# Kernel optimization log

Measured on AMD Instinct MI355X. Metric: run time of the kernel, lower is better.

## Reference

```python
import jax, jax.numpy as jnp
import numpy as np

N, F, H, D, E, G = 50000, 64, 4, 64, 800000, 64
NEG_SLOPE = 0.2


def setup_inputs() -> dict:
    key = jax.random.key(0)
    ks = jax.random.split(key, 10)
    return {
        "x": jax.random.normal(ks[0], (N, F), jnp.float32),
        "mask": jax.random.uniform(ks[1], (N, F), jnp.float32),
        "edge_index": jax.random.randint(ks[2], (2, E), 0, N, jnp.int64),
        "batch_idx": jnp.sort(jax.random.randint(ks[3], (N,), 0, G, jnp.int64)),
        "W_gat": jax.random.normal(ks[4], (H * D, F), jnp.float32) * 0.05,
        "att_src": jax.random.normal(ks[5], (H, D), jnp.float32) * 0.05,
        "att_dst": jax.random.normal(ks[6], (H, D), jnp.float32) * 0.05,
        "bias_gat": jax.random.normal(ks[7], (H * D,), jnp.float32) * 0.05,
        "W_lin": jax.random.normal(ks[8], (D, H * D), jnp.float32) * 0.05,
        "b_lin": jax.random.normal(ks[9], (D,), jnp.float32) * 0.05,
    }


def reference(x, mask, edge_index, batch_idx, W_gat, att_src, att_dst, bias_gat, W_lin, b_lin):
    n = x.shape[0]
    row, col = edge_index[0], edge_index[1]

    # ---- get_mask(mask, edge_index, hops=1): scatter_add(mask[col] -> row), threshold
    m = jax.ops.segment_sum(mask[col], row, num_segments=n)
    m = (m > 0).astype(x.dtype)  # [N, F]

    # ---- GATConv(x, edge_index): add self loops (PyG default)
    loop = jnp.arange(n, dtype=edge_index.dtype)
    src = jnp.concatenate([edge_index[0], loop])  # source j
    dst = jnp.concatenate([edge_index[1], loop])  # target i

    xw = (x @ W_gat.T).reshape(n, H, D)  # per-head projection [N,H,D]
    a_s = jnp.einsum("nhd,hd->nh", xw, att_src)  # [N,H]
    a_d = jnp.einsum("nhd,hd->nh", xw, att_dst)
    e = jax.nn.leaky_relu(a_s[src] + a_d[dst], NEG_SLOPE)  # [E+N, H]

    # segment softmax over incoming edges of each destination node
    emax = jax.ops.segment_max(e, dst, num_segments=n)  # [N,H]
    ex = jnp.exp(e - emax[dst])
    denom = jax.ops.segment_sum(ex, dst, num_segments=n)
    alpha = ex / (denom[dst] + 1e-16)  # [E+N, H]

    out = jax.ops.segment_sum(alpha[:, :, None] * xw[src], dst, num_segments=n)
    out = out.reshape(n, H * D) + bias_gat  # concat heads + bias

    # ---- mask expand to heads and fuse: x = linear(x * mask)
    mexp = jnp.broadcast_to(m[:, None, :], (n, H, F)).reshape(n, H * F)
    out = (out * mexp) @ W_lin.T + b_lin  # [N, D]

    # ---- GraphSizeNorm: divide by sqrt(#nodes in each graph)
    deg = jax.ops.segment_sum(jnp.ones((n,), x.dtype), batch_idx, num_segments=G)
    inv_sqrt = jnp.where(deg > 0, deg, 1.0) ** -0.5
    out = out * inv_sqrt[batch_idx][:, None]
    return out
```

## Files before the change

kernel.cpp:

```cpp
#include <hip/hip_runtime.h>
#include <cstdint>
#include <math.h>

constexpr float NEG_SLOPE = 0.2f;

__device__ __forceinline__ float lrelu(float v) { return v > 0.0f ? v : NEG_SLOPE * v; }

__device__ __forceinline__ unsigned short f2bf(float f) {
    uint32_t u = __float_as_uint(f);
    uint32_t r = (u + 0x7fffu + ((u >> 16) & 1u)) >> 16;
    return (unsigned short)r;
}
__device__ __forceinline__ float bf2f(unsigned short v) { return __uint_as_float((uint32_t)v << 16); }
__device__ __forceinline__ float bflo(uint32_t v) { return __uint_as_float(v << 16); }
__device__ __forceinline__ float bfhi(uint32_t v) { return __uint_as_float(v & 0xffff0000u); }

typedef short bf16x8 __attribute__((ext_vector_type(8)));
typedef float f32x4 __attribute__((ext_vector_type(4)));

__launch_bounds__(256)
__global__ void k_att2z(const float* __restrict__ x, const float* __restrict__ Wg,
                        const float* __restrict__ att_s, const float* __restrict__ att_d,
                        float* __restrict__ a_s, float* __restrict__ a_d,
                        int* __restrict__ deg, unsigned long long* __restrict__ magg,
                        int* __restrict__ startg, int N)
{
    __shared__ float vs_l[256];
    __shared__ float vd_l[256];
    int tid = threadIdx.x;
    {
        int h = tid >> 6, k = tid & 63;
        float s = 0.f, d = 0.f;
        for (int dd = 0; dd < 64; ++dd) {
            float w = Wg[(size_t)(h * 64 + dd) * 64 + k];
            s += w * att_s[h * 64 + dd];
            d += w * att_d[h * 64 + dd];
        }
        vs_l[tid] = s; vd_l[tid] = d;
    }
    if (blockIdx.x == 0 && tid < 64) startg[tid] = N;
    __syncthreads();
    int i = blockIdx.x * 256 + tid;
    if (i >= N) return;
    deg[i] = 0; magg[i] = 0ULL;
    const float4* xr = (const float4*)(x + (size_t)i * 64);
    float s0=0,s1=0,s2=0,s3=0, d0=0,d1=0,d2=0,d3=0;
    #pragma unroll
    for (int q = 0; q < 16; ++q) {
        float4 xv = xr[q];
        float4 a0 = *(const float4*)&vs_l[4*q];
        float4 a1 = *(const float4*)&vs_l[64 + 4*q];
        float4 a2 = *(const float4*)&vs_l[128 + 4*q];
        float4 a3 = *(const float4*)&vs_l[192 + 4*q];
        float4 c0 = *(const float4*)&vd_l[4*q];
        float4 c1 = *(const float4*)&vd_l[64 + 4*q];
        float4 c2 = *(const float4*)&vd_l[128 + 4*q];
        float4 c3 = *(const float4*)&vd_l[192 + 4*q];
        s0 += xv.x*a0.x + xv.y*a0.y + xv.z*a0.z + xv.w*a0.w;
        s1 += xv.x*a1.x + xv.y*a1.y + xv.z*a1.z + xv.w*a1.w;
        s2 += xv.x*a2.x + xv.y*a2.y + xv.z*a2.z + xv.w*a2.w;
        s3 += xv.x*a3.x + xv.y*a3.y + xv.z*a3.z + xv.w*a3.w;
        d0 += xv.x*c0.x + xv.y*c0.y + xv.z*c0.z + xv.w*c0.w;
        d1 += xv.x*c1.x + xv.y*c1.y + xv.z*c1.z + xv.w*c1.w;
        d2 += xv.x*c2.x + xv.y*c2.y + xv.z*c2.z + xv.w*c2.w;
        d3 += xv.x*c3.x + xv.y*c3.y + xv.z*c3.z + xv.w*c3.w;
    }
    *(float4*)&a_s[(size_t)i * 4] = make_float4(s0, s1, s2, s3);
    *(float4*)&a_d[(size_t)i * 4] = make_float4(d0, d1, d2, d3);
}

__global__ void k_maskdeg(const float* __restrict__ mask, const int* __restrict__ ei,
                          unsigned long long* __restrict__ mbits, int* __restrict__ deg,
                          int N, int E, int nbMask)
{
    int tid = threadIdx.x;
    if ((int)blockIdx.x < nbMask) {
        int wid  = (blockIdx.x * 256 + tid) >> 6;
        int lane = tid & 63;
        if (wid >= N) return;
        float v = mask[(size_t)wid * 64 + lane];
        unsigned long long b = __ballot(v > 0.0f);
        if (lane == 0) mbits[wid] = b;
    } else {
        int e = (blockIdx.x - nbMask) * 256 + tid;
        if (e >= E) return;
        atomicAdd(deg + ei[E + e], 1);
    }
}

__launch_bounds__(256)
__global__ void k_gemm1m(const float* __restrict__ x, const float* __restrict__ Wg,
                         const int* __restrict__ batch_idx,
                         uint32_t* __restrict__ xwp, int* __restrict__ startg, int N)
{
    __shared__ __align__(16) uint32_t AsH[2048];
    __shared__ __align__(16) uint32_t AsL[2048];
    __shared__ __align__(16) uint32_t BsH[8192];
    const int tid = threadIdx.x;
    const int r0  = blockIdx.x * 64;

    for (int idx = tid; idx < 2048; idx += 256) {
        int r = idx >> 5, k2 = idx & 31;
        float2 v = make_float2(0.f, 0.f);
        if (r0 + r < N) v = *(const float2*)&x[(size_t)(r0 + r) * 64 + 2 * k2];
        unsigned short h0 = f2bf(v.x), h1 = f2bf(v.y);
        unsigned short l0 = f2bf(v.x - bf2f(h0)), l1 = f2bf(v.y - bf2f(h1));
        int di = (r * 32 + k2) ^ ((r & 7) << 2);
        AsH[di] = (uint32_t)h0 | ((uint32_t)h1 << 16);
        AsL[di] = (uint32_t)l0 | ((uint32_t)l1 << 16);
    }
    for (int idx = tid; idx < 8192; idx += 256) {
        int c = idx >> 5, k2 = idx & 31;
        float2 v = *(const float2*)&Wg[(size_t)c * 64 + 2 * k2];
        int di = (c * 32 + k2) ^ ((c & 7) << 2);
        BsH[di] = (uint32_t)f2bf(v.x) | ((uint32_t)f2bf(v.y) << 16);
    }
    if (tid < 64 && (r0 + tid) < N) {
        int i = r0 + tid;
        int b = batch_idx[i];
        int pb = (i > 0) ? batch_idx[i - 1] : -1;
        if (b != pb) startg[b] = i;
    }
    __syncthreads();

    const int lane = tid & 63;
    const int wv   = tid >> 6;
    const int rl   = lane & 15;
    const int kg   = lane >> 4;
    const int ct0  = (wv & 1) * 2 + (wv >> 1) * 8;
    const int swz  = (rl & 7) << 2;

    f32x4 acc[4][4];
    #pragma unroll
    for (int r = 0; r < 4; ++r)
        #pragma unroll
        for (int cs = 0; cs < 4; ++cs) acc[r][cs] = (f32x4){0.f, 0.f, 0.f, 0.f};

    #pragma unroll
    for (int ks = 0; ks < 2; ++ks) {
        bf16x8 aH[4], aL[4], bH[4];
        #pragma unroll
        for (int r = 0; r < 4; ++r) {
            int ui = (((r * 16 + rl) * 32) + ks * 16 + kg * 4) ^ swz;
            aH[r] = *(const bf16x8*)&AsH[ui];
            aL[r] = *(const bf16x8*)&AsL[ui];
        }
        #pragma unroll
        for (int cs = 0; cs < 4; ++cs) {
            int ct = ct0 + (cs & 1) + (cs >> 1) * 4;
            int ui = (((ct * 16 + rl) * 32) + ks * 16 + kg * 4) ^ swz;
            bH[cs] = *(const bf16x8*)&BsH[ui];
        }
        #pragma unroll
        for (int r = 0; r < 4; ++r)
            #pragma unroll
            for (int cs = 0; cs < 4; ++cs) {
                acc[r][cs] = __builtin_amdgcn_mfma_f32_16x16x32_bf16(aH[r], bH[cs], acc[r][cs], 0, 0, 0);
                acc[r][cs] = __builtin_amdgcn_mfma_f32_16x16x32_bf16(aL[r], bH[cs], acc[r][cs], 0, 0, 0);
            }
    }

    #pragma unroll
    for (int r = 0; r < 4; ++r) {
        #pragma unroll
        for (int reg = 0; reg < 4; ++reg) {
            int row = r0 + r * 16 + kg * 4 + reg;
            if (row < N) {
                #pragma unroll
                for (int p = 0; p < 2; ++p) {
                    int c_lo = (ct0 + p) * 16 + rl;
                    int wrd  = ((c_lo >> 7) << 6) | (c_lo & 63);
                    uint32_t lo = f2bf(acc[r][p][reg]);
                    uint32_t hi = f2bf(acc[r][p + 2][reg]);
                    xwp[(size_t)row * 128 + wrd] = lo | (hi << 16);
                }
            }
        }
    }
}

__global__ void k_scan1(const int* __restrict__ deg, int* __restrict__ off,
                        int* __restrict__ bsum, int N)
{
    __shared__ int s[256];
    int t = threadIdx.x;
    int i = blockIdx.x * 256 + t;
    int v = (i < N) ? deg[i] : 0;
    s[t] = v; __syncthreads();
    for (int o = 1; o < 256; o <<= 1) {
        int u = (t >= o) ? s[t - o] : 0;
        __syncthreads();
        s[t] += u;
        __syncthreads();
    }
    int incl = s[t];
    if (i < N) off[i] = incl - v;
    if (t == 255) bsum[blockIdx.x] = incl;
}

__global__ void k_scan2(const int* __restrict__ bsum, int* __restrict__ bpre,
                        int* __restrict__ off, const int* __restrict__ startg,
                        float* __restrict__ invs, int NB, int N)
{
    __shared__ int s[256];
    int t = threadIdx.x;
    int v = (t < NB) ? bsum[t] : 0;
    s[t] = v; __syncthreads();
    for (int o = 1; o < 256; o <<= 1) {
        int u = (t >= o) ? s[t - o] : 0;
        __syncthreads();
        s[t] += u;
        __syncthreads();
    }
    if (t < NB) bpre[t] = s[t] - v;
    if (t == 255) off[N] = s[255];
    if (t < 64) {
        int st = startg[t];
        int en = N;
        for (int g2 = t + 1; g2 < 64; ++g2) en = min(en, startg[g2]);
        int d = en - st;
        float dv = (d > 0) ? (float)d : 1.0f;
        invs[t] = 1.0f / sqrtf(dv);
    }
}

__global__ void k_scan3(int* __restrict__ off, int* __restrict__ cursor,
                        const int* __restrict__ bpre, int N)
{
    int i = blockIdx.x * blockDim.x + threadIdx.x;
    if (i >= N) return;
    int v = off[i] + bpre[blockIdx.x];
    off[i] = v;
    cursor[i] = v;
}

__global__ void k_fill(const int* __restrict__ ei, int* __restrict__ cursor,
                       int* __restrict__ csr,
                       const unsigned long long* __restrict__ mbits,
                       unsigned long long* __restrict__ magg, int E)
{
    int e = blockIdx.x * blockDim.x + threadIdx.x;
    if (e >= E) return;
    int r = ei[e];
    int c = ei[E + e];
    unsigned long long b = mbits[c];
    if ((magg[r] & b) != b) atomicOr(magg + r, b);
    int pos = atomicAdd(cursor + c, 1);
    csr[pos] = r;
}

__launch_bounds__(256)
__global__ void k_main7(const uint32_t* __restrict__ xwp,
                        const float* __restrict__ a_s,
                        const float* __restrict__ a_d,
                        const int* __restrict__ off,
                        const int* __restrict__ csr,
                        const unsigned long long* __restrict__ magg,
                        const float* __restrict__ bias,
                        uint32_t* __restrict__ tbp, int N)
{
    __shared__ __align__(16) uint32_t su[4][64];
    __shared__ __align__(16) float2 e01s[4][64];
    __shared__ __align__(16) float2 e23s[4][64];

    const int lane = threadIdx.x & 63;
    const int wv   = threadIdx.x >> 6;
    const int wid  = blockIdx.x * 4 + wv;
    const int nw   = gridDim.x * 4;
    const int hp   = lane >> 5;
    const int d0   = (lane & 31) * 2;

    const uint2* xw2 = (const uint2*)xwp;
    const float2 bsL = *(const float2*)&bias[hp * 128 + d0];
    const float2 bsH = *(const float2*)&bias[hp * 128 + 64 + d0];
    const float2* ep = hp ? e23s[wv] : e01s[wv];

    for (int i = wid; i < N; i += nw) {
        const int beg = off[i], end = off[i + 1];
        const float4 adv = *(const float4*)(a_d + (size_t)i * 4);
        const float4 asv = *(const float4*)(a_s + (size_t)i * 4);
        const float ex0 = __expf(lrelu(asv.x + adv.x));
        const float ex1 = __expf(lrelu(asv.y + adv.y));
        const float ex2 = __expf(lrelu(asv.z + adv.z));
        const float ex3 = __expf(lrelu(asv.w + adv.w));

        const uint2 sv = xw2[(size_t)i * 64 + lane];
        const float wls = hp ? ex2 : ex0;
        const float whs = hp ? ex3 : ex1;
        float accL0 = wls * bflo(sv.x), accH0 = whs * bfhi(sv.x);
        float accL1 = wls * bflo(sv.y), accH1 = whs * bfhi(sv.y);
        float sL = 0.f, sH = 0.f;

        for (int kc = beg; kc < end; kc += 64) {
            const int cnt = min(64, end - kc);
            uint32_t sreg = 0; float e0 = 0.f, e1 = 0.f, e2 = 0.f, e3 = 0.f;
            if (lane < cnt) {
                sreg = csr[kc + lane];
                const float4 g = *(const float4*)(a_s + (size_t)sreg * 4);
                e0 = __expf(lrelu(g.x + adv.x));
                e1 = __expf(lrelu(g.y + adv.y));
                e2 = __expf(lrelu(g.z + adv.z));
                e3 = __expf(lrelu(g.w + adv.w));
            }
            su[wv][lane]   = sreg;
            e01s[wv][lane] = make_float2(e0, e1);
            e23s[wv][lane] = make_float2(e2, e3);

            int j = 0;
            for (; j + 8 <= cnt; j += 8) {
                uint4 sq0 = *(const uint4*)&su[wv][j];
                uint4 sq1 = *(const uint4*)&su[wv][j + 4];
                float2 w0 = ep[j],   w1 = ep[j+1], w2 = ep[j+2], w3 = ep[j+3];
                float2 w4 = ep[j+4], w5 = ep[j+5], w6 = ep[j+6], w7 = ep[j+7];
                uint2 v0 = xw2[(size_t)sq0.x * 64 + lane];
                uint2 v1 = xw2[(size_t)sq0.y * 64 + lane];
                uint2 v2 = xw2[(size_t)sq0.z * 64 + lane];
                uint2 v3 = xw2[(size_t)sq0.w * 64 + lane];
                uint2 v4 = xw2[(size_t)sq1.x * 64 + lane];
                uint2 v5 = xw2[(size_t)sq1.y * 64 + lane];
                uint2 v6 = xw2[(size_t)sq1.z * 64 + lane];
                uint2 v7 = xw2[(size_t)sq1.w * 64 + lane];
                sL += w0.x + w1.x + w2.x + w3.x + w4.x + w5.x + w6.x + w7.x;
                sH += w0.y + w1.y + w2.y + w3.y + w4.y + w5.y + w6.y + w7.y;
                accL0 += w0.x * bflo(v0.x); accH0 += w0.y * bfhi(v0.x);
                accL1 += w0.x * bflo(v0.y); accH1 += w0.y * bfhi(v0.y);
                accL0 += w1.x * bflo(v1.x); accH0 += w1.y * bfhi(v1.x);
                accL1 += w1.x * bflo(v1.y); accH1 += w1.y * bfhi(v1.y);
                accL0 += w2.x * bflo(v2.x); accH0 += w2.y * bfhi(v2.x);
                accL1 += w2.x * bflo(v2.y); accH1 += w2.y * bfhi(v2.y);
                accL0 += w3.x * bflo(v3.x); accH0 += w3.y * bfhi(v3.x);
                accL1 += w3.x * bflo(v3.y); accH1 += w3.y * bfhi(v3.y);
                accL0 += w4.x * bflo(v4.x); accH0 += w4.y * bfhi(v4.x);
                accL1 += w4.x * bflo(v4.y); accH1 += w4.y * bfhi(v4.y);
                accL0 += w5.x * bflo(v5.x); accH0 += w5.y * bfhi(v5.x);
                accL1 += w5.x * bflo(v5.y); accH1 += w5.y * bfhi(v5.y);
                accL0 += w6.x * bflo(v6.x); accH0 += w6.y * bfhi(v6.x);
                accL1 += w6.x * bflo(v6.y); accH1 += w6.y * bfhi(v6.y);
                accL0 += w7.x * bflo(v7.x); accH0 += w7.y * bfhi(v7.x);
                accL1 += w7.x * bflo(v7.y); accH1 += w7.y * bfhi(v7.y);
            }
            for (; j + 4 <= cnt; j += 4) {
                uint4 sq = *(const uint4*)&su[wv][j];
                float2 wA = ep[j], wB = ep[j+1], wC = ep[j+2], wD = ep[j+3];
                uint2 vA = xw2[(size_t)sq.x * 64 + lane];
                uint2 vB = xw2[(size_t)sq.y * 64 + lane];
                uint2 vC = xw2[(size_t)sq.z * 64 + lane];
                uint2 vD = xw2[(size_t)sq.w * 64 + lane];
                sL += wA.x + wB.x + wC.x + wD.x;
                sH += wA.y + wB.y + wC.y + wD.y;
                accL0 += wA.x * bflo(vA.x); accH0 += wA.y * bfhi(vA.x);
                accL1 += wA.x * bflo(vA.y); accH1 += wA.y * bfhi(vA.y);
                accL0 += wB.x * bflo(vB.x); accH0 += wB.y * bfhi(vB.x);
                accL1 += wB.x * bflo(vB.y); accH1 += wB.y * bfhi(vB.y);
                accL0 += wC.x * bflo(vC.x); accH0 += wC.y * bfhi(vC.x);
                accL1 += wC.x * bflo(vC.y); accH1 += wC.y * bfhi(vC.y);
                accL0 += wD.x * bflo(vD.x); accH0 += wD.y * bfhi(vD.x);
                accL1 += wD.x * bflo(vD.y); accH1 += wD.y * bfhi(vD.y);
            }
            for (; j < cnt; ++j) {
                uint32_t s = su[wv][j];
                float2 wE = ep[j];
                uint2 v = xw2[(size_t)s * 64 + lane];
                sL += wE.x; sH += wE.y;
                accL0 += wE.x * bflo(v.x); accH0 += wE.y * bfhi(v.x);
                accL1 += wE.x * bflo(v.y); accH1 += wE.y * bfhi(v.y);
            }
        }
        const float rlo = 1.0f / (sL + wls + 1e-16f);
        const float rhi = 1.0f / (sH + whs + 1e-16f);

        const unsigned long long mb = magg[i];
        const float m0 = (float)((mb >> d0) & 1ULL);
        const float m1 = (float)((mb >> (d0 + 1)) & 1ULL);
        float oL0 = (accL0 * rlo + bsL.x) * m0, oL1 = (accL1 * rlo + bsL.y) * m1;
        float oH0 = (accH0 * rhi + bsH.x) * m0, oH1 = (accH1 * rhi + bsH.y) * m1;
        tbp[(size_t)i * 128 + hp * 64 + (lane & 31)]      = (uint32_t)f2bf(oL0) | ((uint32_t)f2bf(oL1) << 16);
        tbp[(size_t)i * 128 + hp * 64 + 32 + (lane & 31)] = (uint32_t)f2bf(oH0) | ((uint32_t)f2bf(oH1) << 16);
    }
}

__launch_bounds__(256)
__global__ void k_gemm2m(const uint32_t* __restrict__ tbp, const float* __restrict__ Wl,
                         const float* __restrict__ bl,
                         const int* __restrict__ batch_idx, const float* __restrict__ invs,
                         float* __restrict__ out, int N)
{
    __shared__ __align__(16) uint32_t AH[2048];
    __shared__ __align__(16) uint32_t BH[2048];
    __shared__ __align__(16) uint32_t BL[2048];
    const int tid = threadIdx.x;
    const int r0  = blockIdx.x * 64;
    const int lane = tid & 63;
    const int wv   = tid >> 6;
    const int rl   = lane & 15;
    const int kg   = lane >> 4;
    const int swz  = (rl & 7) << 2;

    f32x4 acc[4];
    #pragma unroll
    for (int r = 0; r < 4; ++r) acc[r] = (f32x4){0.f, 0.f, 0.f, 0.f};

    for (int kc = 0; kc < 4; ++kc) {
        if (kc) __syncthreads();
        for (int idx = tid; idx < 2048; idx += 256) {
            int r = idx >> 5, k2 = idx & 31;
            uint32_t v = 0;
            if (r0 + r < N) v = tbp[(size_t)(r0 + r) * 128 + kc * 32 + k2];
            AH[(r * 32 + k2) ^ ((r & 7) << 2)] = v;
        }
        for (int idx = tid; idx < 2048; idx += 256) {
            int c = idx >> 5, k2 = idx & 31;
            float2 v = *(const float2*)&Wl[(size_t)c * 256 + kc * 64 + 2 * k2];
            unsigned short h0 = f2bf(v.x), h1 = f2bf(v.y);
            unsigned short l0 = f2bf(v.x - bf2f(h0)), l1 = f2bf(v.y - bf2f(h1));
            int di = (c * 32 + k2) ^ ((c & 7) << 2);
            BH[di] = (uint32_t)h0 | ((uint32_t)h1 << 16);
            BL[di] = (uint32_t)l0 | ((uint32_t)l1 << 16);
        }
        __syncthreads();

        #pragma unroll
        for (int ks = 0; ks < 2; ++ks) {
            int uib = ((wv * 16 + rl) * 32 + ks * 16 + kg * 4) ^ swz;
            bf16x8 bHf = *(const bf16x8*)&BH[uib];
            bf16x8 bLf = *(const bf16x8*)&BL[uib];
            #pragma unroll
            for (int r = 0; r < 4; ++r) {
                int ui = ((r * 16 + rl) * 32 + ks * 16 + kg * 4) ^ swz;
                bf16x8 aHf = *(const bf16x8*)&AH[ui];
                acc[r] = __builtin_amdgcn_mfma_f32_16x16x32_bf16(aHf, bHf, acc[r], 0, 0, 0);
                acc[r] = __builtin_amdgcn_mfma_f32_16x16x32_bf16(aHf, bLf, acc[r], 0, 0, 0);
            }
        }
    }

    const int col = wv * 16 + rl;
    const float blc = bl[col];
    #pragma unroll
    for (int r = 0; r < 4; ++r) {
        #pragma unroll
        for (int reg = 0; reg < 4; ++reg) {
            int row = r0 + r * 16 + kg * 4 + reg;
            if (row < N) {
                float sc = invs[batch_idx[row]];
                out[(size_t)row * 64 + col] = (acc[r][reg] + blc) * sc;
            }
        }
    }
}

extern "C" void kernel_launch(void* const* d_in, const int* in_sizes, int n_in,
                              void* d_out, int out_size, void* d_ws, size_t ws_size,
                              hipStream_t stream)
{
    const float* x      = (const float*)d_in[0];
    const float* mask   = (const float*)d_in[1];
    const int*   ei     = (const int*)d_in[2];
    const int*   batch  = (const int*)d_in[3];
    const float* Wg     = (const float*)d_in[4];
    const float* att_s  = (const float*)d_in[5];
    const float* att_d  = (const float*)d_in[6];
    const float* bias_g = (const float*)d_in[7];
    const float* Wl     = (const float*)d_in[8];
    const float* bl     = (const float*)d_in[9];
    float* out = (float*)d_out;

    const int N = in_sizes[0] / 64;
    const int E = in_sizes[2] / 2;

    char* w = (char*)d_ws;
    auto alloc = [&](size_t bytes) { char* p = w; w += (bytes + 255) & ~(size_t)255; return p; };
    uint32_t* xwp  = (uint32_t*)alloc((size_t)N * 128 * 4);
    uint32_t* tbp  = (uint32_t*)alloc((size_t)N * 128 * 4);
    float* a_s   = (float*)alloc((size_t)N * 4 * 4);
    float* a_d   = (float*)alloc((size_t)N * 4 * 4);
    unsigned long long* mbits = (unsigned long long*)alloc((size_t)N * 8);
    unsigned long long* magg  = (unsigned long long*)alloc((size_t)N * 8);
    int* deg    = (int*)alloc((size_t)N * 4);
    int* off    = (int*)alloc((size_t)(N + 1) * 4);
    int* cursor = (int*)alloc((size_t)N * 4);
    int* csr    = (int*)alloc((size_t)E * 4);
    int* bsum   = (int*)alloc(256 * 4);
    int* bpre   = (int*)alloc(256 * 4);
    int* startg = (int*)alloc(64 * 4);
    float* invs = (float*)alloc(64 * 4);

    int nbN4  = (N + 3) / 4;
    int nbE   = (E + 255) / 256;
    int nb256 = (N + 255) / 256;

    k_att2z<<<nb256, 256, 0, stream>>>(x, Wg, att_s, att_d, a_s, a_d, deg, magg, startg, N);
    k_maskdeg<<<nbN4 + nbE, 256, 0, stream>>>(mask, ei, mbits, deg, N, E, nbN4);
    k_gemm1m<<<(N + 63) / 64, 256, 0, stream>>>(x, Wg, batch, xwp, startg, N);
    k_scan1<<<nb256, 256, 0, stream>>>(deg, off, bsum, N);
    k_scan2<<<1, 256, 0, stream>>>(bsum, bpre, off, startg, invs, nb256, N);
    k_scan3<<<nb256, 256, 0, stream>>>(off, cursor, bpre, N);
    k_fill<<<nbE, 256, 0, stream>>>(ei, cursor, csr, mbits, magg, E);
    k_main7<<<2048, 256, 0, stream>>>(xwp, a_s, a_d, off, csr, magg, bias_g, tbp, N);
    k_gemm2m<<<(N + 63) / 64, 256, 0, stream>>>(tbp, Wl, bl, batch, invs, out, N);
}
```

Baseline: 234.6 us.

## Precompute bf16 weights once and fold attention logits into first GEMM

```diff
diff --git a/kernel.cpp b/kernel.cpp
--- a/kernel.cpp
+++ b/kernel.cpp
@@ -18,17 +18,30 @@
 typedef short bf16x8 __attribute__((ext_vector_type(8)));
 typedef float f32x4 __attribute__((ext_vector_type(4)));
 
-__launch_bounds__(256)
-__global__ void k_att2z(const float* __restrict__ x, const float* __restrict__ Wg,
+__global__ void k_wprep(const float* __restrict__ Wg, const float* __restrict__ Wl,
                         const float* __restrict__ att_s, const float* __restrict__ att_d,
-                        float* __restrict__ a_s, float* __restrict__ a_d,
-                        int* __restrict__ deg, unsigned long long* __restrict__ magg,
+                        uint32_t* __restrict__ WgB, uint32_t* __restrict__ WlH,
+                        uint32_t* __restrict__ WlL, uint32_t* __restrict__ attB,
                         int* __restrict__ startg, int N)
 {
-    __shared__ float vs_l[256];
-    __shared__ float vd_l[256];
-    int tid = threadIdx.x;
-    {
+    const int tid = threadIdx.x;
+    if (blockIdx.x == 0) {
+        for (int w = tid; w < 8192; w += 256) {
+            int c = w >> 5, k2 = w & 31;
+            float2 v = *(const float2*)&Wg[(size_t)c * 64 + 2 * k2];
+            WgB[w] = (uint32_t)f2bf(v.x) | ((uint32_t)f2bf(v.y) << 16);
+        }
+    } else if (blockIdx.x == 1) {
+        for (int w = tid; w < 8192; w += 256) {
+            int c = w >> 7, k2 = w & 127;
+            float2 v = *(const float2*)&Wl[(size_t)c * 256 + 2 * k2];
+            unsigned short h0 = f2bf(v.x), h1 = f2bf(v.y);
+            unsigned short l0 = f2bf(v.x - bf2f(h0)), l1 = f2bf(v.y - bf2f(h1));
+            WlH[w] = (uint32_t)h0 | ((uint32_t)h1 << 16);
+            WlL[w] = (uint32_t)l0 | ((uint32_t)l1 << 16);
+        }
+    } else {
+        __shared__ float vs_l[256], vd_l[256];
         int h = tid >> 6, k = tid & 63;
         float s = 0.f, d = 0.f;
         for (int dd = 0; dd < 64; ++dd) {
@@ -37,36 +50,20 @@
             d += w * att_d[h * 64 + dd];
         }
         vs_l[tid] = s; vd_l[tid] = d;
-    }
-    if (blockIdx.x == 0 && tid < 64) startg[tid] = N;
-    __syncthreads();
-    int i = blockIdx.x * 256 + tid;
-    if (i >= N) return;
-    deg[i] = 0; magg[i] = 0ULL;
-    const float4* xr = (const float4*)(x + (size_t)i * 64);
-    float s0=0,s1=0,s2=0,s3=0, d0=0,d1=0,d2=0,d3=0;
-    #pragma unroll
-    for (int q = 0; q < 16; ++q) {
-        float4 xv = xr[q];
-        float4 a0 = *(const float4*)&vs_l[4*q];
-        float4 a1 = *(const float4*)&vs_l[64 + 4*q];
-        float4 a2 = *(const float4*)&vs_l[128 + 4*q];
-        float4 a3 = *(const float4*)&vs_l[192 + 4*q];
-        float4 c0 = *(const float4*)&vd_l[4*q];
-        float4 c1 = *(const float4*)&vd_l[64 + 4*q];
-        float4 c2 = *(const float4*)&vd_l[128 + 4*q];
-        float4 c3 = *(const float4*)&vd_l[192 + 4*q];
-        s0 += xv.x*a0.x + xv.y*a0.y + xv.z*a0.z + xv.w*a0.w;
-        s1 += xv.x*a1.x + xv.y*a1.y + xv.z*a1.z + xv.w*a1.w;
-        s2 += xv.x*a2.x + xv.y*a2.y + xv.z*a2.z + xv.w*a2.w;
-        s3 += xv.x*a3.x + xv.y*a3.y + xv.z*a3.z + xv.w*a3.w;
-        d0 += xv.x*c0.x + xv.y*c0.y + xv.z*c0.z + xv.w*c0.w;
-        d1 += xv.x*c1.x + xv.y*c1.y + xv.z*c1.z + xv.w*c1.w;
-        d2 += xv.x*c2.x + xv.y*c2.y + xv.z*c2.z + xv.w*c2.w;
-        d3 += xv.x*c3.x + xv.y*c3.y + xv.z*c3.z + xv.w*c3.w;
-    }
-    *(float4*)&a_s[(size_t)i * 4] = make_float4(s0, s1, s2, s3);
-    *(float4*)&a_d[(size_t)i * 4] = make_float4(d0, d1, d2, d3);
+        if (tid < 64) startg[tid] = N;
+        __syncthreads();
+        for (int w = tid; w < 512; w += 256) {
+            int col = w >> 5, k2 = w & 31;
+            int hh = col & 3;
+            int plane = (col >> 2) & 1;
+            const float* buf = (col >> 3) ? vd_l : vs_l;
+            float v0 = buf[hh * 64 + 2 * k2];
+            float v1 = buf[hh * 64 + 2 * k2 + 1];
+            unsigned short h0 = f2bf(v0), h1 = f2bf(v1);
+            if (plane) { h0 = f2bf(v0 - bf2f(h0)); h1 = f2bf(v1 - bf2f(h1)); }
+            attB[w] = (uint32_t)h0 | ((uint32_t)h1 << 16);
+        }
+    }
 }
 
 __global__ void k_maskdeg(const float* __restrict__ mask, const int* __restrict__ ei,
@@ -89,13 +86,13 @@
 }
 
 __launch_bounds__(256)
-__global__ void k_gemm1m(const float* __restrict__ x, const float* __restrict__ Wg,
-                         const int* __restrict__ batch_idx,
-                         uint32_t* __restrict__ xwp, int* __restrict__ startg, int N)
+__global__ void k_gemm1n(const float* __restrict__ x, const uint32_t* __restrict__ WgB,
+                         const uint32_t* __restrict__ attB, const int* __restrict__ batch_idx,
+                         uint32_t* __restrict__ xwp, float* __restrict__ a_s,
+                         float* __restrict__ a_d, int* __restrict__ startg, int N)
 {
     __shared__ __align__(16) uint32_t AsH[2048];
     __shared__ __align__(16) uint32_t AsL[2048];
-    __shared__ __align__(16) uint32_t BsH[8192];
     const int tid = threadIdx.x;
     const int r0  = blockIdx.x * 64;
 
@@ -109,12 +106,6 @@
         AsH[di] = (uint32_t)h0 | ((uint32_t)h1 << 16);
         AsL[di] = (uint32_t)l0 | ((uint32_t)l1 << 16);
     }
-    for (int idx = tid; idx < 8192; idx += 256) {
-        int c = idx >> 5, k2 = idx & 31;
-        float2 v = *(const float2*)&Wg[(size_t)c * 64 + 2 * k2];
-        int di = (c * 32 + k2) ^ ((c & 7) << 2);
-        BsH[di] = (uint32_t)f2bf(v.x) | ((uint32_t)f2bf(v.y) << 16);
-    }
     if (tid < 64 && (r0 + tid) < N) {
         int i = r0 + tid;
         int b = batch_idx[i];
@@ -135,6 +126,7 @@
     for (int r = 0; r < 4; ++r)
         #pragma unroll
         for (int cs = 0; cs < 4; ++cs) acc[r][cs] = (f32x4){0.f, 0.f, 0.f, 0.f};
+    f32x4 accA = (f32x4){0.f, 0.f, 0.f, 0.f};
 
     #pragma unroll
     for (int ks = 0; ks < 2; ++ks) {
@@ -148,9 +140,9 @@
         #pragma unroll
         for (int cs = 0; cs < 4; ++cs) {
             int ct = ct0 + (cs & 1) + (cs >> 1) * 4;
-            int ui = (((ct * 16 + rl) * 32) + ks * 16 + kg * 4) ^ swz;
-            bH[cs] = *(const bf16x8*)&BsH[ui];
-        }
+            bH[cs] = *(const bf16x8*)(WgB + ((ct * 16 + rl) * 32 + ks * 16 + kg * 4));
+        }
+        bf16x8 bAtt = *(const bf16x8*)(attB + (rl * 32 + ks * 16 + kg * 4));
         #pragma unroll
         for (int r = 0; r < 4; ++r)
             #pragma unroll
@@ -158,6 +150,8 @@
                 acc[r][cs] = __builtin_amdgcn_mfma_f32_16x16x32_bf16(aH[r], bH[cs], acc[r][cs], 0, 0, 0);
                 acc[r][cs] = __builtin_amdgcn_mfma_f32_16x16x32_bf16(aL[r], bH[cs], acc[r][cs], 0, 0, 0);
             }
+        accA = __builtin_amdgcn_mfma_f32_16x16x32_bf16(aH[wv], bAtt, accA, 0, 0, 0);
+        accA = __builtin_amdgcn_mfma_f32_16x16x32_bf16(aL[wv], bAtt, accA, 0, 0, 0);
     }
 
     #pragma unroll
@@ -175,6 +169,15 @@
                     xwp[(size_t)row * 128 + wrd] = lo | (hi << 16);
                 }
             }
+        }
+    }
+    #pragma unroll
+    for (int reg = 0; reg < 4; ++reg) {
+        float v = accA[reg] + __shfl_xor(accA[reg], 4);
+        int row = r0 + wv * 16 + kg * 4 + reg;
+        if (row < N) {
+            if (rl < 4)                a_s[(size_t)row * 4 + rl]       = v;
+            else if (rl >= 8 && rl < 12) a_d[(size_t)row * 4 + (rl - 8)] = v;
         }
     }
 }
@@ -380,61 +383,43 @@
 }
 
 __launch_bounds__(256)
-__global__ void k_gemm2m(const uint32_t* __restrict__ tbp, const float* __restrict__ Wl,
-                         const float* __restrict__ bl,
+__global__ void k_gemm2n(const uint32_t* __restrict__ tbp, const uint32_t* __restrict__ WlH,
+                         const uint32_t* __restrict__ WlL, const float* __restrict__ bl,
                          const int* __restrict__ batch_idx, const float* __restrict__ invs,
                          float* __restrict__ out, int N)
 {
-    __shared__ __align__(16) uint32_t AH[2048];
-    __shared__ __align__(16) uint32_t BH[2048];
-    __shared__ __align__(16) uint32_t BL[2048];
     const int tid = threadIdx.x;
     const int r0  = blockIdx.x * 64;
     const int lane = tid & 63;
     const int wv   = tid >> 6;
     const int rl   = lane & 15;
     const int kg   = lane >> 4;
-    const int swz  = (rl & 7) << 2;
+    const int col  = wv * 16 + rl;
 
     f32x4 acc[4];
     #pragma unroll
     for (int r = 0; r < 4; ++r) acc[r] = (f32x4){0.f, 0.f, 0.f, 0.f};
 
+    const uint32_t* wbH = WlH + col * 128;
+    const uint32_t* wbL = WlL + col * 128;
+
     for (int kc = 0; kc < 4; ++kc) {
-        if (kc) __syncthreads();
-        for (int idx = tid; idx < 2048; idx += 256) {
-            int r = idx >> 5, k2 = idx & 31;
-            uint32_t v = 0;
-            if (r0 + r < N) v = tbp[(size_t)(r0 + r) * 128 + kc * 32 + k2];
-            AH[(r * 32 + k2) ^ ((r & 7) << 2)] = v;
-        }
-        for (int idx = tid; idx < 2048; idx += 256) {
-            int c = idx >> 5, k2 = idx & 31;
-            float2 v = *(const float2*)&Wl[(size_t)c * 256 + kc * 64 + 2 * k2];
-            unsigned short h0 = f2bf(v.x), h1 = f2bf(v.y);
-            unsigned short l0 = f2bf(v.x - bf2f(h0)), l1 = f2bf(v.y - bf2f(h1));
-            int di = (c * 32 + k2) ^ ((c & 7) << 2);
-            BH[di] = (uint32_t)h0 | ((uint32_t)h1 << 16);
-            BL[di] = (uint32_t)l0 | ((uint32_t)l1 << 16);
-        }
-        __syncthreads();
-
         #pragma unroll
         for (int ks = 0; ks < 2; ++ks) {
-            int uib = ((wv * 16 + rl) * 32 + ks * 16 + kg * 4) ^ swz;
-            bf16x8 bHf = *(const bf16x8*)&BH[uib];
-            bf16x8 bLf = *(const bf16x8*)&BL[uib];
+            const int wo = kc * 32 + ks * 16 + kg * 4;
+            bf16x8 bHf = *(const bf16x8*)(wbH + wo);
+            bf16x8 bLf = *(const bf16x8*)(wbL + wo);
             #pragma unroll
             for (int r = 0; r < 4; ++r) {
-                int ui = ((r * 16 + rl) * 32 + ks * 16 + kg * 4) ^ swz;
-                bf16x8 aHf = *(const bf16x8*)&AH[ui];
+                int row = r0 + r * 16 + rl;
+                bf16x8 aHf = (bf16x8){0,0,0,0,0,0,0,0};
+                if (row < N) aHf = *(const bf16x8*)(tbp + (size_t)row * 128 + wo);
                 acc[r] = __builtin_amdgcn_mfma_f32_16x16x32_bf16(aHf, bHf, acc[r], 0, 0, 0);
                 acc[r] = __builtin_amdgcn_mfma_f32_16x16x32_bf16(aHf, bLf, acc[r], 0, 0, 0);
             }
         }
     }
 
-    const int col = wv * 16 + rl;
     const float blc = bl[col];
     #pragma unroll
     for (int r = 0; r < 4; ++r) {
@@ -484,18 +469,24 @@
     int* bpre   = (int*)alloc(256 * 4);
     int* startg = (int*)alloc(64 * 4);
     float* invs = (float*)alloc(64 * 4);
+    uint32_t* WgB  = (uint32_t*)alloc(8192 * 4);
+    uint32_t* WlH  = (uint32_t*)alloc(8192 * 4);
+    uint32_t* WlL  = (uint32_t*)alloc(8192 * 4);
+    uint32_t* attB = (uint32_t*)alloc(512 * 4);
 
     int nbN4  = (N + 3) / 4;
     int nbE   = (E + 255) / 256;
     int nb256 = (N + 255) / 256;
 
-    k_att2z<<<nb256, 256, 0, stream>>>(x, Wg, att_s, att_d, a_s, a_d, deg, magg, startg, N);
+    hipMemsetAsync(deg, 0, (size_t)N * 4, stream);
+    hipMemsetAsync(magg, 0, (size_t)N * 8, stream);
+    k_wprep<<<3, 256, 0, stream>>>(Wg, Wl, att_s, att_d, WgB, WlH, WlL, attB, startg, N);
     k_maskdeg<<<nbN4 + nbE, 256, 0, stream>>>(mask, ei, mbits, deg, N, E, nbN4);
-    k_gemm1m<<<(N + 63) / 64, 256, 0, stream>>>(x, Wg, batch, xwp, startg, N);
+    k_gemm1n<<<(N + 63) / 64, 256, 0, stream>>>(x, WgB, attB, batch, xwp, a_s, a_d, startg, N);
     k_scan1<<<nb256, 256, 0, stream>>>(deg, off, bsum, N);
     k_scan2<<<1, 256, 0, stream>>>(bsum, bpre, off, startg, invs, nb256, N);
     k_scan3<<<nb256, 256, 0, stream>>>(off, cursor, bpre, N);
     k_fill<<<nbE, 256, 0, stream>>>(ei, cursor, csr, mbits, magg, E);
     k_main7<<<2048, 256, 0, stream>>>(xwp, a_s, a_d, off, csr, magg, bias_g, tbp, N);
-    k_gemm2m<<<(N + 63) / 64, 256, 0, stream>>>(tbp, Wl, bl, batch, invs, out, N);
-}
+    k_gemm2n<<<(N + 63) / 64, 256, 0, stream>>>(tbp, WlH, WlL, bl, batch, invs, out, N);
+}
```

After: 249.4 us. 1.06x slower.

## Fuse attention score projection into the first GEMM via extra MFMA columns

Applied to the files above, without the earlier changes.

```diff
diff --git a/kernel.cpp b/kernel.cpp
--- a/kernel.cpp
+++ b/kernel.cpp
@@ -18,63 +18,41 @@
 typedef short bf16x8 __attribute__((ext_vector_type(8)));
 typedef float f32x4 __attribute__((ext_vector_type(4)));
 
-__launch_bounds__(256)
-__global__ void k_att2z(const float* __restrict__ x, const float* __restrict__ Wg,
-                        const float* __restrict__ att_s, const float* __restrict__ att_d,
-                        float* __restrict__ a_s, float* __restrict__ a_d,
-                        int* __restrict__ deg, unsigned long long* __restrict__ magg,
-                        int* __restrict__ startg, int N)
-{
-    __shared__ float vs_l[256];
-    __shared__ float vd_l[256];
-    int tid = threadIdx.x;
-    {
-        int h = tid >> 6, k = tid & 63;
-        float s = 0.f, d = 0.f;
-        for (int dd = 0; dd < 64; ++dd) {
-            float w = Wg[(size_t)(h * 64 + dd) * 64 + k];
-            s += w * att_s[h * 64 + dd];
-            d += w * att_d[h * 64 + dd];
-        }
-        vs_l[tid] = s; vd_l[tid] = d;
-    }
-    if (blockIdx.x == 0 && tid < 64) startg[tid] = N;
+__global__ void k_wprep1(const float* __restrict__ Wg,
+                         const float* __restrict__ att_s, const float* __restrict__ att_d,
+                         uint32_t* __restrict__ attB)
+{
+    __shared__ float vs_l[256], vd_l[256];
+    const int tid = threadIdx.x;
+    int h = tid >> 6, k = tid & 63;
+    float s = 0.f, d = 0.f;
+    for (int dd = 0; dd < 64; ++dd) {
+        float w = Wg[(size_t)(h * 64 + dd) * 64 + k];
+        s += w * att_s[h * 64 + dd];
+        d += w * att_d[h * 64 + dd];
+    }
+    vs_l[tid] = s; vd_l[tid] = d;
     __syncthreads();
-    int i = blockIdx.x * 256 + tid;
-    if (i >= N) return;
-    deg[i] = 0; magg[i] = 0ULL;
-    const float4* xr = (const float4*)(x + (size_t)i * 64);
-    float s0=0,s1=0,s2=0,s3=0, d0=0,d1=0,d2=0,d3=0;
-    #pragma unroll
-    for (int q = 0; q < 16; ++q) {
-        float4 xv = xr[q];
-        float4 a0 = *(const float4*)&vs_l[4*q];
-        float4 a1 = *(const float4*)&vs_l[64 + 4*q];
-        float4 a2 = *(const float4*)&vs_l[128 + 4*q];
-        float4 a3 = *(const float4*)&vs_l[192 + 4*q];
-        float4 c0 = *(const float4*)&vd_l[4*q];
-        float4 c1 = *(const float4*)&vd_l[64 + 4*q];
-        float4 c2 = *(const float4*)&vd_l[128 + 4*q];
-        float4 c3 = *(const float4*)&vd_l[192 + 4*q];
-        s0 += xv.x*a0.x + xv.y*a0.y + xv.z*a0.z + xv.w*a0.w;
-        s1 += xv.x*a1.x + xv.y*a1.y + xv.z*a1.z + xv.w*a1.w;
-        s2 += xv.x*a2.x + xv.y*a2.y + xv.z*a2.z + xv.w*a2.w;
-        s3 += xv.x*a3.x + xv.y*a3.y + xv.z*a3.z + xv.w*a3.w;
-        d0 += xv.x*c0.x + xv.y*c0.y + xv.z*c0.z + xv.w*c0.w;
-        d1 += xv.x*c1.x + xv.y*c1.y + xv.z*c1.z + xv.w*c1.w;
-        d2 += xv.x*c2.x + xv.y*c2.y + xv.z*c2.z + xv.w*c2.w;
-        d3 += xv.x*c3.x + xv.y*c3.y + xv.z*c3.z + xv.w*c3.w;
-    }
-    *(float4*)&a_s[(size_t)i * 4] = make_float4(s0, s1, s2, s3);
-    *(float4*)&a_d[(size_t)i * 4] = make_float4(d0, d1, d2, d3);
+    for (int w = tid; w < 512; w += 256) {
+        int col = w >> 5, k2 = w & 31;
+        int hh = col & 3;
+        int plane = (col >> 2) & 1;
+        const float* buf = (col >> 3) ? vd_l : vs_l;
+        float v0 = buf[hh * 64 + 2 * k2];
+        float v1 = buf[hh * 64 + 2 * k2 + 1];
+        unsigned short h0 = f2bf(v0), h1 = f2bf(v1);
+        if (plane) { h0 = f2bf(v0 - bf2f(h0)); h1 = f2bf(v1 - bf2f(h1)); }
+        attB[w] = (uint32_t)h0 | ((uint32_t)h1 << 16);
+    }
 }
 
 __global__ void k_maskdeg(const float* __restrict__ mask, const int* __restrict__ ei,
                           unsigned long long* __restrict__ mbits, int* __restrict__ deg,
-                          int N, int E, int nbMask)
+                          int* __restrict__ startg, int N, int E, int nbMask)
 {
     int tid = threadIdx.x;
     if ((int)blockIdx.x < nbMask) {
+        if (blockIdx.x == 0 && tid < 64) startg[tid] = N;
         int wid  = (blockIdx.x * 256 + tid) >> 6;
         int lane = tid & 63;
         if (wid >= N) return;
@@ -89,9 +67,10 @@
 }
 
 __launch_bounds__(256)
-__global__ void k_gemm1m(const float* __restrict__ x, const float* __restrict__ Wg,
-                         const int* __restrict__ batch_idx,
-                         uint32_t* __restrict__ xwp, int* __restrict__ startg, int N)
+__global__ void k_gemm1m_att(const float* __restrict__ x, const float* __restrict__ Wg,
+                             const uint32_t* __restrict__ attB, const int* __restrict__ batch_idx,
+                             uint32_t* __restrict__ xwp, float* __restrict__ a_s,
+                             float* __restrict__ a_d, int* __restrict__ startg, int N)
 {
     __shared__ __align__(16) uint32_t AsH[2048];
     __shared__ __align__(16) uint32_t AsL[2048];
@@ -135,6 +114,7 @@
     for (int r = 0; r < 4; ++r)
         #pragma unroll
         for (int cs = 0; cs < 4; ++cs) acc[r][cs] = (f32x4){0.f, 0.f, 0.f, 0.f};
+    f32x4 accA = (f32x4){0.f, 0.f, 0.f, 0.f};
 
     #pragma unroll
     for (int ks = 0; ks < 2; ++ks) {
@@ -151,6 +131,7 @@
             int ui = (((ct * 16 + rl) * 32) + ks * 16 + kg * 4) ^ swz;
             bH[cs] = *(const bf16x8*)&BsH[ui];
         }
+        bf16x8 bAtt = *(const bf16x8*)(attB + (rl * 32 + ks * 16 + kg * 4));
         #pragma unroll
         for (int r = 0; r < 4; ++r)
             #pragma unroll
@@ -158,6 +139,8 @@
                 acc[r][cs] = __builtin_amdgcn_mfma_f32_16x16x32_bf16(aH[r], bH[cs], acc[r][cs], 0, 0, 0);
                 acc[r][cs] = __builtin_amdgcn_mfma_f32_16x16x32_bf16(aL[r], bH[cs], acc[r][cs], 0, 0, 0);
             }
+        accA = __builtin_amdgcn_mfma_f32_16x16x32_bf16(aH[wv], bAtt, accA, 0, 0, 0);
+        accA = __builtin_amdgcn_mfma_f32_16x16x32_bf16(aL[wv], bAtt, accA, 0, 0, 0);
     }
 
     #pragma unroll
@@ -175,6 +158,15 @@
                     xwp[(size_t)row * 128 + wrd] = lo | (hi << 16);
                 }
             }
+        }
+    }
+    #pragma unroll
+    for (int reg = 0; reg < 4; ++reg) {
+        float v = accA[reg] + __shfl_xor(accA[reg], 4);
+        int row = r0 + wv * 16 + kg * 4 + reg;
+        if (row < N) {
+            if (rl < 4)                  a_s[(size_t)row * 4 + rl]       = v;
+            else if (rl >= 8 && rl < 12) a_d[(size_t)row * 4 + (rl - 8)] = v;
         }
     }
 }
@@ -484,14 +476,17 @@
     int* bpre   = (int*)alloc(256 * 4);
     int* startg = (int*)alloc(64 * 4);
     float* invs = (float*)alloc(64 * 4);
+    uint32_t* attB = (uint32_t*)alloc(512 * 4);
 
     int nbN4  = (N + 3) / 4;
     int nbE   = (E + 255) / 256;
     int nb256 = (N + 255) / 256;
 
-    k_att2z<<<nb256, 256, 0, stream>>>(x, Wg, att_s, att_d, a_s, a_d, deg, magg, startg, N);
-    k_maskdeg<<<nbN4 + nbE, 256, 0, stream>>>(mask, ei, mbits, deg, N, E, nbN4);
-    k_gemm1m<<<(N + 63) / 64, 256, 0, stream>>>(x, Wg, batch, xwp, startg, N);
+    hipMemsetAsync(deg, 0, (size_t)N * 4, stream);
+    hipMemsetAsync(magg, 0, (size_t)N * 8, stream);
+    k_wprep1<<<1, 256, 0, stream>>>(Wg, att_s, att_d, attB);
+    k_maskdeg<<<nbN4 + nbE, 256, 0, stream>>>(mask, ei, mbits, deg, startg, N, E, nbN4);
+    k_gemm1m_att<<<(N + 63) / 64, 256, 0, stream>>>(x, Wg, attB, batch, xwp, a_s, a_d, startg, N);
     k_scan1<<<nb256, 256, 0, stream>>>(deg, off, bsum, N);
     k_scan2<<<1, 256, 0, stream>>>(bsum, bpre, off, startg, invs, nb256, N);
     k_scan3<<<nb256, 256, 0, stream>>>(off, cursor, bpre, N);
```

Result: slower. 256.7 us (+9.4%).
